# Kernel optimization log

Hardware: AMD Instinct MI355X
Metric: run time of the kernel (lower is better)

The kernel has to match this reference:

```python
import jax, jax.numpy as jnp
import numpy as np

N_HOPS = 3
VOCAB, D = 100000, 300
B, S, T = 128, 2048, 4
N_CLASSES = 3


def setup_inputs() -> dict:
    key = jax.random.key(0)
    ks = jax.random.split(key, 9)
    return {
        "inputs": jax.random.randint(ks[0], (B, S), 0, VOCAB, dtype=jnp.int64 if jax.config.jax_enable_x64 else jnp.int32),
        "targets": jax.random.randint(ks[1], (B, T), 0, VOCAB, dtype=jnp.int64 if jax.config.jax_enable_x64 else jnp.int32),
        "emb_table": jax.random.normal(ks[2], (VOCAB, D), dtype=jnp.float32) * 0.1,
        "W_att": jax.random.normal(ks[3], (2 * D, 1), dtype=jnp.float32) * 0.05,
        "b_att": jax.random.normal(ks[4], (1,), dtype=jnp.float32) * 0.05,
        "W_tr": jax.random.normal(ks[5], (D, D), dtype=jnp.float32) * 0.05,
        "b_tr": jax.random.normal(ks[6], (D,), dtype=jnp.float32) * 0.05,
        "W_out": jax.random.normal(ks[7], (D, N_CLASSES), dtype=jnp.float32) * 0.05,
        "b_out": jax.random.normal(ks[8], (N_CLASSES,), dtype=jnp.float32) * 0.05,
    }


def reference(inputs, targets, emb_table, W_att, b_att, W_tr, b_tr, W_out, b_out):
    # Embedding lookups (dropout prob = 0.0 -> identity)
    we = emb_table[inputs]    # [B, S, D] word/context embeddings
    te = emb_table[targets]   # [B, T, D] aspect-term embeddings
    d = we.shape[-1]
    # Split concat-linear: cat([we, u]) @ W_att == we @ Wa + u @ Wu (avoids [B,S,2D] intermediate)
    Wa, Wu = W_att[:d], W_att[d:]          # each [D, 1]
    u = jnp.mean(te, axis=1, keepdims=True)  # [B, 1, D]
    for _ in range(N_HOPS):
        g = jnp.tanh(we @ Wa + u @ Wu + b_att)          # [B, S, 1]
        a = jax.nn.softmax(g, axis=1)                    # softmax over sequence
        vec = jnp.einsum('bs,bsd->bd', a[..., 0], we)    # [B, D] attention-weighted sum
        te = vec[:, None, :] + te @ W_tr + b_tr          # [B, T, D] (broadcast add)
        u = jnp.mean(te, axis=1, keepdims=True)          # [B, 1, D]
    return u[:, 0, :] @ W_out + b_out                    # [B, n_classes]
```

## Files before the change

### kernel.cpp

```cpp
#include <hip/hip_runtime.h>
#include <hip/hip_bf16.h>

#define VOCAB 100000
#define D 300
#define B 128
#define S 2048
#define T 4

#define WS_V      0
#define WS_WTWU   3600
#define WS_WT2WU  3900
#define WS_WTWO   4200
#define WS_W2WO   5100
#define WS_WT3WO  6000
#define WS_CONST  6900
#define WS_DSCAL  6916
#define WS_PROJ   7940


__device__ __forceinline__ float wave_red(float x) {
    #pragma unroll
    for (int m = 1; m < 64; m <<= 1) x += __shfl_xor(x, m, 64);
    return x;
}

__global__ __launch_bounds__(64) void k_derive1(const float* __restrict__ Watt,
                                                const float* __restrict__ Wtr,
                                                const float* __restrict__ Wout,
                                                float* __restrict__ ws) {
    int i = blockIdx.x, lane = threadIdx.x;
    const float* wrow = Wtr + (size_t)i * D;
    float au = 0.f, a0 = 0.f, a1 = 0.f, a2 = 0.f;
    for (int j = lane; j < D; j += 64) {
        float w = wrow[j];
        au += w * Watt[D + j];
        a0 += w * Wout[j * 3 + 0];
        a1 += w * Wout[j * 3 + 1];
        a2 += w * Wout[j * 3 + 2];
    }
    au = wave_red(au); a0 = wave_red(a0); a1 = wave_red(a1); a2 = wave_red(a2);
    if (lane == 0) {
        ws[WS_WTWU + i] = au;
        ws[WS_WTWO + i * 3 + 0] = a0;
        ws[WS_WTWO + i * 3 + 1] = a1;
        ws[WS_WTWO + i * 3 + 2] = a2;
    }
}

__global__ __launch_bounds__(64) void k_derive2(const float* __restrict__ Wtr,
                                                float* __restrict__ ws) {
    int i = blockIdx.x, lane = threadIdx.x;
    const float* wrow = Wtr + (size_t)i * D;
    float au = 0.f, a0 = 0.f, a1 = 0.f, a2 = 0.f;
    for (int j = lane; j < D; j += 64) {
        float w = wrow[j];
        au += w * ws[WS_WTWU + j];
        a0 += w * ws[WS_WTWO + j * 3 + 0];
        a1 += w * ws[WS_WTWO + j * 3 + 1];
        a2 += w * ws[WS_WTWO + j * 3 + 2];
    }
    au = wave_red(au); a0 = wave_red(a0); a1 = wave_red(a1); a2 = wave_red(a2);
    if (lane == 0) {
        ws[WS_WT2WU + i] = au;
        ws[WS_W2WO + i * 3 + 0] = a0;
        ws[WS_W2WO + i * 3 + 1] = a1;
        ws[WS_W2WO + i * 3 + 2] = a2;
    }
}

__global__ __launch_bounds__(64) void k_derive3(const float* __restrict__ Watt,
                                                const float* __restrict__ Wtr,
                                                const float* __restrict__ Wout,
                                                float* __restrict__ ws) {
    int i = blockIdx.x, lane = threadIdx.x;
    const float* wrow = Wtr + (size_t)i * D;
    float a0 = 0.f, a1 = 0.f, a2 = 0.f;
    for (int j = lane; j < D; j += 64) {
        float w = wrow[j];
        a0 += w * ws[WS_W2WO + j * 3 + 0];
        a1 += w * ws[WS_W2WO + j * 3 + 1];
        a2 += w * ws[WS_W2WO + j * 3 + 2];
    }
    a0 = wave_red(a0); a1 = wave_red(a1); a2 = wave_red(a2);
    if (lane == 0) {
        ws[WS_WT3WO + i * 3 + 0] = a0;
        ws[WS_WT3WO + i * 3 + 1] = a1;
        ws[WS_WT3WO + i * 3 + 2] = a2;
    }
    if (lane < 12) {
        float val;
        if      (lane == 0) val = Watt[i];
        else if (lane == 1) val = Watt[D + i];
        else if (lane == 2) val = ws[WS_WTWU + i];
        else if (lane < 6)  val = Wout[i * 3 + (lane - 3)];
        else if (lane < 9)  val = ws[WS_WTWO + i * 3 + (lane - 6)];
        else                val = ws[WS_W2WO + i * 3 + (lane - 9)];
        ws[WS_V + i * 12 + lane] = val;
    }
}

__global__ __launch_bounds__(64) void k_small(const int* __restrict__ targets,
                                              const float* __restrict__ E,
                                              const float* __restrict__ Watt,
                                              const float* __restrict__ Wout,
                                              const float* __restrict__ btr,
                                              float* __restrict__ ws) {
    int lane = threadIdx.x;
    if (blockIdx.x < B) {
        int b = blockIdx.x;
        int t0 = targets[b * T + 0], t1 = targets[b * T + 1];
        int t2 = targets[b * T + 2], t3 = targets[b * T + 3];
        const float* r0 = E + (size_t)t0 * D;
        const float* r1 = E + (size_t)t1 * D;
        const float* r2 = E + (size_t)t2 * D;
        const float* r3 = E + (size_t)t3 * D;
        float a0 = 0.f, a1 = 0.f, a2 = 0.f, a3 = 0.f, a4 = 0.f, a5 = 0.f;
        for (int i = lane; i < D; i += 64) {
            float u = 0.25f * (r0[i] + r1[i] + r2[i] + r3[i]);
            a0 += u * Watt[D + i];
            a1 += u * ws[WS_WTWU + i];
            a2 += u * ws[WS_WT2WU + i];
            a3 += u * ws[WS_WT3WO + i * 3 + 0];
            a4 += u * ws[WS_WT3WO + i * 3 + 1];
            a5 += u * ws[WS_WT3WO + i * 3 + 2];
        }
        a0 = wave_red(a0); a1 = wave_red(a1); a2 = wave_red(a2);
        a3 = wave_red(a3); a4 = wave_red(a4); a5 = wave_red(a5);
        if (lane == 0) {
            float* o = ws + WS_DSCAL + b * 8;
            o[0] = a0; o[1] = a1; o[2] = a2; o[3] = a3; o[4] = a4; o[5] = a5;
        }
    } else {
        float acc[11];
        #pragma unroll
        for (int k = 0; k < 11; ++k) acc[k] = 0.f;
        for (int i = lane; i < D; i += 64) {
            float bt = btr[i];
            acc[0] += bt * Watt[D + i];
            acc[1] += bt * ws[WS_WTWU + i];
            acc[2] += bt * Wout[i * 3 + 0];
            acc[3] += bt * Wout[i * 3 + 1];
            acc[4] += bt * Wout[i * 3 + 2];
            acc[5] += bt * ws[WS_WTWO + i * 3 + 0];
            acc[6] += bt * ws[WS_WTWO + i * 3 + 1];
            acc[7] += bt * ws[WS_WTWO + i * 3 + 2];
            acc[8] += bt * ws[WS_W2WO + i * 3 + 0];
            acc[9] += bt * ws[WS_W2WO + i * 3 + 1];
            acc[10] += bt * ws[WS_W2WO + i * 3 + 2];
        }
        #pragma unroll
        for (int k = 0; k < 11; ++k) acc[k] = wave_red(acc[k]);
        if (lane == 0) {
            #pragma unroll
            for (int k = 0; k < 11; ++k) ws[WS_CONST + k] = acc[k];
        }
    }
}

__global__ __launch_bounds__(256) void k_proj(const float* __restrict__ E,
                                              const float* __restrict__ Vg,
                                              float* __restrict__ proj) {
    int lane = threadIdx.x & 63;
    int wid  = (blockIdx.x * blockDim.x + threadIdx.x) >> 6;
    int row  = wid * 64 + lane;
    if (row >= VOCAB) return;

    const float4* er = (const float4*)(E + (size_t)row * D);
    float acc[12];
    #pragma unroll
    for (int c = 0; c < 12; ++c) acc[c] = 0.f;

    #pragma unroll 5
    for (int k4 = 0; k4 < 75; ++k4) {
        float4 e = er[k4];
        const float* vp = Vg + k4 * 48;
        #pragma unroll
        for (int c = 0; c < 12; ++c) {
            acc[c] += e.x * vp[c];
            acc[c] += e.y * vp[12 + c];
            acc[c] += e.z * vp[24 + c];
            acc[c] += e.w * vp[36 + c];
        }
    }

    float4* dst = (float4*)(proj + (size_t)row * 12);
    dst[0] = make_float4(acc[0], acc[1], acc[2],  acc[3]);
    dst[1] = make_float4(acc[4], acc[5], acc[6],  acc[7]);
    dst[2] = make_float4(acc[8], acc[9], acc[10], acc[11]);
}

__global__ __launch_bounds__(1024) void k_hops(const int* __restrict__ inputs,
                                               const float* __restrict__ ws,
                                               const float* __restrict__ batt,
                                               const float* __restrict__ bout,
                                               float* __restrict__ out) {
    __shared__ float wred[16][13];
    __shared__ float Ash[13];
    __shared__ float sc[4];
    int b = blockIdx.x, tid = threadIdx.x, wave = tid >> 6, lane = tid & 63;
    const float* proj = ws + WS_PROJ;
    const float* cst  = ws + WS_CONST;
    const float* dsc  = ws + WS_DSCAL + b * 8;
    const int*   inp  = inputs + (size_t)b * S;

    float pv[2][12];
    #pragma unroll
    for (int q = 0; q < 2; ++q) {
        int s = tid + 1024 * q;
        int idx = inp[s];
        const float4* pr = (const float4*)(proj + (size_t)idx * 12);
        float4 x = pr[0], y = pr[1], z = pr[2];
        pv[q][0] = x.x; pv[q][1] = x.y; pv[q][2]  = x.z; pv[q][3]  = x.w;
        pv[q][4] = y.x; pv[q][5] = y.y; pv[q][6]  = y.z; pv[q][7]  = y.w;
        pv[q][8] = z.x; pv[q][9] = z.y; pv[q][10] = z.z; pv[q][11] = z.w;
    }

    if (tid == 0) sc[0] = dsc[0] + batt[0];
    __syncthreads();
    float c = sc[0];

    float o3c0 = 0.f, o3c1 = 0.f, o3c2 = 0.f, uWtWu = 0.f;

    #pragma unroll
    for (int hop = 0; hop < 3; ++hop) {
        float acc[12];
        #pragma unroll
        for (int k = 0; k < 12; ++k) acc[k] = 0.f;
        #pragma unroll
        for (int q = 0; q < 2; ++q) {
            float g = tanhf(pv[q][0] + c);
            float e = __expf(g);
            acc[11] += e;
            #pragma unroll
            for (int k = 1; k < 12; ++k) acc[k - 1] += e * pv[q][k];
        }
        #pragma unroll
        for (int m = 1; m < 64; m <<= 1) {
            #pragma unroll
            for (int k = 0; k < 12; ++k) acc[k] += __shfl_xor(acc[k], m, 64);
        }
        if (lane == 0) {
            #pragma unroll
            for (int k = 0; k < 12; ++k) wred[wave][k] = acc[k];
        }
        __syncthreads();
        if (tid < 12) {
            float s = 0.f;
            #pragma unroll
            for (int w = 0; w < 16; ++w) s += wred[w][tid];
            Ash[tid] = s;
        }
        __syncthreads();
        if (tid == 0) {
            float inv = 1.0f / Ash[11];
            if (hop == 0) {
                o3c0  = Ash[8] * inv + dsc[3] + cst[8];
                o3c1  = Ash[9] * inv + dsc[4] + cst[9];
                o3c2  = Ash[10] * inv + dsc[5] + cst[10];
                uWtWu = Ash[1] * inv + dsc[2] + cst[1];
                sc[0] = Ash[0] * inv + dsc[1] + cst[0] + batt[0];
            } else if (hop == 1) {
                o3c0  = Ash[5] * inv + o3c0 + cst[5];
                o3c1  = Ash[6] * inv + o3c1 + cst[6];
                o3c2  = Ash[7] * inv + o3c2 + cst[7];
                sc[0] = Ash[0] * inv + uWtWu + cst[0] + batt[0];
            } else {
                out[b * 3 + 0] = Ash[2] * inv + o3c0 + cst[2] + bout[0];
                out[b * 3 + 1] = Ash[3] * inv + o3c1 + cst[3] + bout[1];
                out[b * 3 + 2] = Ash[4] * inv + o3c2 + cst[4] + bout[2];
            }
        }
        __syncthreads();
        c = sc[0];
    }
}

extern "C" void kernel_launch(void* const* d_in, const int* in_sizes, int n_in,
                              void* d_out, int out_size, void* d_ws, size_t ws_size,
                              hipStream_t stream) {
    const int*   inputs  = (const int*)  d_in[0];
    const int*   targets = (const int*)  d_in[1];
    const float* emb     = (const float*)d_in[2];
    const float* Watt    = (const float*)d_in[3];
    const float* batt    = (const float*)d_in[4];
    const float* Wtr     = (const float*)d_in[5];
    const float* btr     = (const float*)d_in[6];
    const float* Wout    = (const float*)d_in[7];
    const float* bout    = (const float*)d_in[8];
    float* ws  = (float*)d_ws;
    float* out = (float*)d_out;

    hipLaunchKernelGGL(k_derive1, dim3(D),    dim3(64),   0, stream, Watt, Wtr, Wout, ws);
    hipLaunchKernelGGL(k_derive2, dim3(D),    dim3(64),   0, stream, Wtr, ws);
    hipLaunchKernelGGL(k_derive3, dim3(D),    dim3(64),   0, stream, Watt, Wtr, Wout, ws);
    hipLaunchKernelGGL(k_proj,    dim3(391),  dim3(256),  0, stream, emb, ws + WS_V, ws + WS_PROJ);
    hipLaunchKernelGGL(k_small,   dim3(B + 1), dim3(64),  0, stream, targets, emb, Watt, Wout, btr, ws);
    hipLaunchKernelGGL(k_hops,    dim3(B),    dim3(1024), 0, stream, inputs, ws, batt, bout, out);
}
```

Measured before the change: 235.9 us.

## Fuse target-embedding dot products into hop kernel and merge small kernels

```diff
diff --git a/kernel.cpp b/kernel.cpp
--- a/kernel.cpp
+++ b/kernel.cpp
@@ -14,7 +14,6 @@
 #define WS_W2WO   5100
 #define WS_WT3WO  6000
 #define WS_CONST  6900
-#define WS_DSCAL  6916
 #define WS_PROJ   7940
 
 
@@ -22,6 +21,11 @@
     #pragma unroll
     for (int m = 1; m < 64; m <<= 1) x += __shfl_xor(x, m, 64);
     return x;
+}
+
+__device__ __forceinline__ float fast_tanh(float x) {
+    float e = __expf(2.0f * x);
+    return 1.0f - 2.0f / (e + 1.0f);
 }
 
 __global__ __launch_bounds__(64) void k_derive1(const float* __restrict__ Watt,
@@ -47,7 +51,9 @@
     }
 }
 
-__global__ __launch_bounds__(64) void k_derive2(const float* __restrict__ Wtr,
+__global__ __launch_bounds__(64) void k_derive2(const float* __restrict__ Watt,
+                                                const float* __restrict__ Wtr,
+                                                const float* __restrict__ Wout,
                                                 float* __restrict__ ws) {
     int i = blockIdx.x, lane = threadIdx.x;
     const float* wrow = Wtr + (size_t)i * D;
@@ -66,69 +72,41 @@
         ws[WS_W2WO + i * 3 + 1] = a1;
         ws[WS_W2WO + i * 3 + 2] = a2;
     }
+    if (lane < 12) {
+        float val;
+        if      (lane == 0)  val = Watt[i];
+        else if (lane == 1)  val = Watt[D + i];
+        else if (lane == 2)  val = ws[WS_WTWU + i];
+        else if (lane < 6)   val = Wout[i * 3 + (lane - 3)];
+        else if (lane < 9)   val = ws[WS_WTWO + i * 3 + (lane - 6)];
+        else if (lane == 9)  val = a0;
+        else if (lane == 10) val = a1;
+        else                 val = a2;
+        ws[WS_V + i * 12 + lane] = val;
+    }
 }
 
 __global__ __launch_bounds__(64) void k_derive3(const float* __restrict__ Watt,
                                                 const float* __restrict__ Wtr,
                                                 const float* __restrict__ Wout,
+                                                const float* __restrict__ btr,
                                                 float* __restrict__ ws) {
-    int i = blockIdx.x, lane = threadIdx.x;
-    const float* wrow = Wtr + (size_t)i * D;
-    float a0 = 0.f, a1 = 0.f, a2 = 0.f;
-    for (int j = lane; j < D; j += 64) {
-        float w = wrow[j];
-        a0 += w * ws[WS_W2WO + j * 3 + 0];
-        a1 += w * ws[WS_W2WO + j * 3 + 1];
-        a2 += w * ws[WS_W2WO + j * 3 + 2];
-    }
-    a0 = wave_red(a0); a1 = wave_red(a1); a2 = wave_red(a2);
-    if (lane == 0) {
-        ws[WS_WT3WO + i * 3 + 0] = a0;
-        ws[WS_WT3WO + i * 3 + 1] = a1;
-        ws[WS_WT3WO + i * 3 + 2] = a2;
-    }
-    if (lane < 12) {
-        float val;
-        if      (lane == 0) val = Watt[i];
-        else if (lane == 1) val = Watt[D + i];
-        else if (lane == 2) val = ws[WS_WTWU + i];
-        else if (lane < 6)  val = Wout[i * 3 + (lane - 3)];
-        else if (lane < 9)  val = ws[WS_WTWO + i * 3 + (lane - 6)];
-        else                val = ws[WS_W2WO + i * 3 + (lane - 9)];
-        ws[WS_V + i * 12 + lane] = val;
-    }
-}
-
-__global__ __launch_bounds__(64) void k_small(const int* __restrict__ targets,
-                                              const float* __restrict__ E,
-                                              const float* __restrict__ Watt,
-                                              const float* __restrict__ Wout,
-                                              const float* __restrict__ btr,
-                                              float* __restrict__ ws) {
     int lane = threadIdx.x;
-    if (blockIdx.x < B) {
-        int b = blockIdx.x;
-        int t0 = targets[b * T + 0], t1 = targets[b * T + 1];
-        int t2 = targets[b * T + 2], t3 = targets[b * T + 3];
-        const float* r0 = E + (size_t)t0 * D;
-        const float* r1 = E + (size_t)t1 * D;
-        const float* r2 = E + (size_t)t2 * D;
-        const float* r3 = E + (size_t)t3 * D;
-        float a0 = 0.f, a1 = 0.f, a2 = 0.f, a3 = 0.f, a4 = 0.f, a5 = 0.f;
-        for (int i = lane; i < D; i += 64) {
-            float u = 0.25f * (r0[i] + r1[i] + r2[i] + r3[i]);
-            a0 += u * Watt[D + i];
-            a1 += u * ws[WS_WTWU + i];
-            a2 += u * ws[WS_WT2WU + i];
-            a3 += u * ws[WS_WT3WO + i * 3 + 0];
-            a4 += u * ws[WS_WT3WO + i * 3 + 1];
-            a5 += u * ws[WS_WT3WO + i * 3 + 2];
+    if (blockIdx.x < D) {
+        int i = blockIdx.x;
+        const float* wrow = Wtr + (size_t)i * D;
+        float a0 = 0.f, a1 = 0.f, a2 = 0.f;
+        for (int j = lane; j < D; j += 64) {
+            float w = wrow[j];
+            a0 += w * ws[WS_W2WO + j * 3 + 0];
+            a1 += w * ws[WS_W2WO + j * 3 + 1];
+            a2 += w * ws[WS_W2WO + j * 3 + 2];
         }
         a0 = wave_red(a0); a1 = wave_red(a1); a2 = wave_red(a2);
-        a3 = wave_red(a3); a4 = wave_red(a4); a5 = wave_red(a5);
         if (lane == 0) {
-            float* o = ws + WS_DSCAL + b * 8;
-            o[0] = a0; o[1] = a1; o[2] = a2; o[3] = a3; o[4] = a4; o[5] = a5;
+            ws[WS_WT3WO + i * 3 + 0] = a0;
+            ws[WS_WT3WO + i * 3 + 1] = a1;
+            ws[WS_WT3WO + i * 3 + 2] = a2;
         }
     } else {
         float acc[11];
@@ -136,16 +114,16 @@
         for (int k = 0; k < 11; ++k) acc[k] = 0.f;
         for (int i = lane; i < D; i += 64) {
             float bt = btr[i];
-            acc[0] += bt * Watt[D + i];
-            acc[1] += bt * ws[WS_WTWU + i];
-            acc[2] += bt * Wout[i * 3 + 0];
-            acc[3] += bt * Wout[i * 3 + 1];
-            acc[4] += bt * Wout[i * 3 + 2];
-            acc[5] += bt * ws[WS_WTWO + i * 3 + 0];
-            acc[6] += bt * ws[WS_WTWO + i * 3 + 1];
-            acc[7] += bt * ws[WS_WTWO + i * 3 + 2];
-            acc[8] += bt * ws[WS_W2WO + i * 3 + 0];
-            acc[9] += bt * ws[WS_W2WO + i * 3 + 1];
+            acc[0]  += bt * Watt[D + i];
+            acc[1]  += bt * ws[WS_WTWU + i];
+            acc[2]  += bt * Wout[i * 3 + 0];
+            acc[3]  += bt * Wout[i * 3 + 1];
+            acc[4]  += bt * Wout[i * 3 + 2];
+            acc[5]  += bt * ws[WS_WTWO + i * 3 + 0];
+            acc[6]  += bt * ws[WS_WTWO + i * 3 + 1];
+            acc[7]  += bt * ws[WS_WTWO + i * 3 + 2];
+            acc[8]  += bt * ws[WS_W2WO + i * 3 + 0];
+            acc[9]  += bt * ws[WS_W2WO + i * 3 + 1];
             acc[10] += bt * ws[WS_W2WO + i * 3 + 2];
         }
         #pragma unroll
@@ -170,7 +148,7 @@
     #pragma unroll
     for (int c = 0; c < 12; ++c) acc[c] = 0.f;
 
-    #pragma unroll 5
+    #pragma unroll 15
     for (int k4 = 0; k4 < 75; ++k4) {
         float4 e = er[k4];
         const float* vp = Vg + k4 * 48;
@@ -190,17 +168,19 @@
 }
 
 __global__ __launch_bounds__(1024) void k_hops(const int* __restrict__ inputs,
+                                               const int* __restrict__ targets,
+                                               const float* __restrict__ E,
                                                const float* __restrict__ ws,
                                                const float* __restrict__ batt,
                                                const float* __restrict__ bout,
                                                float* __restrict__ out) {
     __shared__ float wred[16][13];
     __shared__ float Ash[13];
+    __shared__ float dsc[8];
     __shared__ float sc[4];
     int b = blockIdx.x, tid = threadIdx.x, wave = tid >> 6, lane = tid & 63;
     const float* proj = ws + WS_PROJ;
     const float* cst  = ws + WS_CONST;
-    const float* dsc  = ws + WS_DSCAL + b * 8;
     const int*   inp  = inputs + (size_t)b * S;
 
     float pv[2][12];
@@ -215,9 +195,74 @@
         pv[q][8] = z.x; pv[q][9] = z.y; pv[q][10] = z.z; pv[q][11] = z.w;
     }
 
-    if (tid == 0) sc[0] = dsc[0] + batt[0];
+    if (wave < 6) {
+        const int* tg = targets + b * T;
+        const float* r0 = E + (size_t)tg[0] * D;
+        const float* r1 = E + (size_t)tg[1] * D;
+        const float* r2 = E + (size_t)tg[2] * D;
+        const float* r3 = E + (size_t)tg[3] * D;
+        const float* vec;
+        int stride3 = 0, col = 0;
+        if      (wave == 0) vec = batt ? nullptr : nullptr;
+        const float* Watt_u = nullptr;
+        float s = 0.f;
+        for (int i = lane; i < D; i += 64) {
+            float u = 0.25f * (r0[i] + r1[i] + r2[i] + r3[i]);
+            float x;
+            if      (wave == 0) x = ws[WS_WTWU - 3600 + 3300 + i];
+            else x = 0.f;
+            (void)x; (void)vec; (void)stride3; (void)col; (void)Watt_u;
+            float v;
+            switch (wave) {
+                case 0: v = *(ws + WS_WTWU + i - 300 + 300); v = 0.f; break;
+                default: v = 0.f;
+            }
+            (void)v;
+            float w;
+            if      (wave == 0) w = ws[3600 + i] * 0.f;
+            else w = 0.f;
+            (void)w;
+            s += 0.f;
+            if      (wave == 0) s += u * ws[WS_WTWU - WS_WTWU + 0];
+            (void)u;
+        }
+        s = 0.f;
+        for (int i = lane; i < D; i += 64) {
+            float u = 0.25f * (r0[i] + r1[i] + r2[i] + r3[i]);
+            float v;
+            if      (wave == 0) v = ws[WS_WTWU + i] * 0.f + *(ws + WS_WTWU + i) * 0.f + 0.f;
+            if      (wave == 0) v = *(E + 0) * 0.f;
+            if      (wave == 0) v = __ldg(ws + WS_WTWU + i) * 0.f;
+            v = 0.f;
+            if      (wave == 0) v = ws[WS_WTWU + i];
+            else if (wave == 1) v = ws[WS_WT2WU + i];
+            else if (wave == 2) v = ws[WS_WT3WO + i * 3 + 0];
+            else if (wave == 3) v = ws[WS_WT3WO + i * 3 + 1];
+            else if (wave == 4) v = ws[WS_WT3WO + i * 3 + 2];
+            else                v = 0.f;
+            s += u * v;
+        }
+        if (wave == 5) {
+            s = 0.f;
+            for (int i = lane; i < D; i += 64) {
+                float u = 0.25f * (r0[i] + r1[i] + r2[i] + r3[i]);
+                s += u * 0.f;
+            }
+        }
+        s = wave_red(s);
+        if (lane == 0) {
+            int slot;
+            if      (wave == 0) slot = 1;
+            else if (wave == 1) slot = 2;
+            else if (wave == 2) slot = 3;
+            else if (wave == 3) slot = 4;
+            else if (wave == 4) slot = 5;
+            else                slot = 0;
+            dsc[slot] = s;
+        }
+    }
     __syncthreads();
-    float c = sc[0];
+    float c = dsc[0] + batt[0];
 
     float o3c0 = 0.f, o3c1 = 0.f, o3c2 = 0.f, uWtWu = 0.f;
 
@@ -228,7 +273,7 @@
         for (int k = 0; k < 12; ++k) acc[k] = 0.f;
         #pragma unroll
         for (int q = 0; q < 2; ++q) {
-            float g = tanhf(pv[q][0] + c);
+            float g = fast_tanh(pv[q][0] + c);
             float e = __expf(g);
             acc[11] += e;
             #pragma unroll
@@ -275,6 +320,116 @@
     }
 }
 
+
+__global__ __launch_bounds__(1024) void k_hops2(const int* __restrict__ inputs,
+                                                const int* __restrict__ targets,
+                                                const float* __restrict__ E,
+                                                const float* __restrict__ Watt,
+                                                const float* __restrict__ ws,
+                                                const float* __restrict__ batt,
+                                                const float* __restrict__ bout,
+                                                float* __restrict__ out) {
+    __shared__ float wred[16][13];
+    __shared__ float Ash[13];
+    __shared__ float dsc[8];
+    __shared__ float sc[4];
+    int b = blockIdx.x, tid = threadIdx.x, wave = tid >> 6, lane = tid & 63;
+    const float* proj = ws + WS_PROJ;
+    const float* cst  = ws + WS_CONST;
+    const int*   inp  = inputs + (size_t)b * S;
+
+    float pv[2][12];
+    #pragma unroll
+    for (int q = 0; q < 2; ++q) {
+        int s = tid + 1024 * q;
+        int idx = inp[s];
+        const float4* pr = (const float4*)(proj + (size_t)idx * 12);
+        float4 x = pr[0], y = pr[1], z = pr[2];
+        pv[q][0] = x.x; pv[q][1] = x.y; pv[q][2]  = x.z; pv[q][3]  = x.w;
+        pv[q][4] = y.x; pv[q][5] = y.y; pv[q][6]  = y.z; pv[q][7]  = y.w;
+        pv[q][8] = z.x; pv[q][9] = z.y; pv[q][10] = z.z; pv[q][11] = z.w;
+    }
+
+    if (wave < 6) {
+        const int* tg = targets + b * T;
+        const float* r0 = E + (size_t)tg[0] * D;
+        const float* r1 = E + (size_t)tg[1] * D;
+        const float* r2 = E + (size_t)tg[2] * D;
+        const float* r3 = E + (size_t)tg[3] * D;
+        float s = 0.f;
+        for (int i = lane; i < D; i += 64) {
+            float u = 0.25f * (r0[i] + r1[i] + r2[i] + r3[i]);
+            float v;
+            if      (wave == 0) v = Watt[D + i];
+            else if (wave == 1) v = ws[WS_WTWU + i];
+            else if (wave == 2) v = ws[WS_WT2WU + i];
+            else if (wave == 3) v = ws[WS_WT3WO + i * 3 + 0];
+            else if (wave == 4) v = ws[WS_WT3WO + i * 3 + 1];
+            else                v = ws[WS_WT3WO + i * 3 + 2];
+            s += u * v;
+        }
+        s = wave_red(s);
+        if (lane == 0) dsc[wave] = s;
+    }
+    __syncthreads();
+    float c = dsc[0] + batt[0];
+
+    float o3c0 = 0.f, o3c1 = 0.f, o3c2 = 0.f, uWtWu = 0.f;
+
+    #pragma unroll
+    for (int hop = 0; hop < 3; ++hop) {
+        float acc[12];
+        #pragma unroll
+        for (int k = 0; k < 12; ++k) acc[k] = 0.f;
+        #pragma unroll
+        for (int q = 0; q < 2; ++q) {
+            float g = fast_tanh(pv[q][0] + c);
+            float e = __expf(g);
+            acc[11] += e;
+            #pragma unroll
+            for (int k = 1; k < 12; ++k) acc[k - 1] += e * pv[q][k];
+        }
+        #pragma unroll
+        for (int m = 1; m < 64; m <<= 1) {
+            #pragma unroll
+            for (int k = 0; k < 12; ++k) acc[k] += __shfl_xor(acc[k], m, 64);
+        }
+        if (lane == 0) {
+            #pragma unroll
+            for (int k = 0; k < 12; ++k) wred[wave][k] = acc[k];
+        }
+        __syncthreads();
+        if (tid < 12) {
+            float s = 0.f;
+            #pragma unroll
+            for (int w = 0; w < 16; ++w) s += wred[w][tid];
+            Ash[tid] = s;
+        }
+        __syncthreads();
+        if (tid == 0) {
+            float inv = 1.0f / Ash[11];
+            if (hop == 0) {
+                o3c0  = Ash[8] * inv + dsc[3] + cst[8];
+                o3c1  = Ash[9] * inv + dsc[4] + cst[9];
+                o3c2  = Ash[10] * inv + dsc[5] + cst[10];
+                uWtWu = Ash[1] * inv + dsc[2] + cst[1];
+                sc[0] = Ash[0] * inv + dsc[1] + cst[0] + batt[0];
+            } else if (hop == 1) {
+                o3c0  = Ash[5] * inv + o3c0 + cst[5];
+                o3c1  = Ash[6] * inv + o3c1 + cst[6];
+                o3c2  = Ash[7] * inv + o3c2 + cst[7];
+                sc[0] = Ash[0] * inv + uWtWu + cst[0] + batt[0];
+            } else {
+                out[b * 3 + 0] = Ash[2] * inv + o3c0 + cst[2] + bout[0];
+                out[b * 3 + 1] = Ash[3] * inv + o3c1 + cst[3] + bout[1];
+                out[b * 3 + 2] = Ash[4] * inv + o3c2 + cst[4] + bout[2];
+            }
+        }
+        __syncthreads();
+        c = sc[0];
+    }
+}
+
 extern "C" void kernel_launch(void* const* d_in, const int* in_sizes, int n_in,
                               void* d_out, int out_size, void* d_ws, size_t ws_size,
                               hipStream_t stream) {
@@ -290,10 +445,10 @@
     float* ws  = (float*)d_ws;
     float* out = (float*)d_out;
 
-    hipLaunchKernelGGL(k_derive1, dim3(D),    dim3(64),   0, stream, Watt, Wtr, Wout, ws);
-    hipLaunchKernelGGL(k_derive2, dim3(D),    dim3(64),   0, stream, Wtr, ws);
-    hipLaunchKernelGGL(k_derive3, dim3(D),    dim3(64),   0, stream, Watt, Wtr, Wout, ws);
-    hipLaunchKernelGGL(k_proj,    dim3(391),  dim3(256),  0, stream, emb, ws + WS_V, ws + WS_PROJ);
-    hipLaunchKernelGGL(k_small,   dim3(B + 1), dim3(64),  0, stream, targets, emb, Watt, Wout, btr, ws);
-    hipLaunchKernelGGL(k_hops,    dim3(B),    dim3(1024), 0, stream, inputs, ws, batt, bout, out);
-}
+    hipLaunchKernelGGL(k_derive1, dim3(D),     dim3(64),   0, stream, Watt, Wtr, Wout, ws);
+    hipLaunchKernelGGL(k_derive2, dim3(D),     dim3(64),   0, stream, Watt, Wtr, Wout, ws);
+    hipLaunchKernelGGL(k_derive3, dim3(D + 1), dim3(64),   0, stream, Watt, Wtr, Wout, btr, ws);
+    hipLaunchKernelGGL(k_proj,    dim3(391),   dim3(256),  0, stream, emb, ws + WS_V, ws + WS_PROJ);
+    hipLaunchKernelGGL(k_hops2,   dim3(B),     dim3(1024), 0, stream, inputs, targets, emb, Watt,
+                       ws, batt, bout, out);
+}
```

Result: slower. 242.9 us (+3.0%).

## Stage embedding tiles in LDS for projection and fold small kernels into neighbors

Applied to the files above, without the earlier changes.

```diff
diff --git a/kernel.cpp b/kernel.cpp
--- a/kernel.cpp
+++ b/kernel.cpp
@@ -14,7 +14,6 @@
 #define WS_W2WO   5100
 #define WS_WT3WO  6000
 #define WS_CONST  6900
-#define WS_DSCAL  6916
 #define WS_PROJ   7940
 
 
@@ -22,6 +21,11 @@
     #pragma unroll
     for (int m = 1; m < 64; m <<= 1) x += __shfl_xor(x, m, 64);
     return x;
+}
+
+__device__ __forceinline__ float fast_tanh(float x) {
+    float e = __expf(2.0f * x);
+    return 1.0f - 2.0f / (e + 1.0f);
 }
 
 __global__ __launch_bounds__(64) void k_derive1(const float* __restrict__ Watt,
@@ -47,7 +51,9 @@
     }
 }
 
-__global__ __launch_bounds__(64) void k_derive2(const float* __restrict__ Wtr,
+__global__ __launch_bounds__(64) void k_derive2(const float* __restrict__ Watt,
+                                                const float* __restrict__ Wtr,
+                                                const float* __restrict__ Wout,
                                                 float* __restrict__ ws) {
     int i = blockIdx.x, lane = threadIdx.x;
     const float* wrow = Wtr + (size_t)i * D;
@@ -66,69 +72,41 @@
         ws[WS_W2WO + i * 3 + 1] = a1;
         ws[WS_W2WO + i * 3 + 2] = a2;
     }
+    if (lane < 12) {
+        float val;
+        if      (lane == 0)  val = Watt[i];
+        else if (lane == 1)  val = Watt[D + i];
+        else if (lane == 2)  val = ws[WS_WTWU + i];
+        else if (lane < 6)   val = Wout[i * 3 + (lane - 3)];
+        else if (lane < 9)   val = ws[WS_WTWO + i * 3 + (lane - 6)];
+        else if (lane == 9)  val = a0;
+        else if (lane == 10) val = a1;
+        else                 val = a2;
+        ws[WS_V + i * 12 + lane] = val;
+    }
 }
 
 __global__ __launch_bounds__(64) void k_derive3(const float* __restrict__ Watt,
                                                 const float* __restrict__ Wtr,
                                                 const float* __restrict__ Wout,
+                                                const float* __restrict__ btr,
                                                 float* __restrict__ ws) {
-    int i = blockIdx.x, lane = threadIdx.x;
-    const float* wrow = Wtr + (size_t)i * D;
-    float a0 = 0.f, a1 = 0.f, a2 = 0.f;
-    for (int j = lane; j < D; j += 64) {
-        float w = wrow[j];
-        a0 += w * ws[WS_W2WO + j * 3 + 0];
-        a1 += w * ws[WS_W2WO + j * 3 + 1];
-        a2 += w * ws[WS_W2WO + j * 3 + 2];
-    }
-    a0 = wave_red(a0); a1 = wave_red(a1); a2 = wave_red(a2);
-    if (lane == 0) {
-        ws[WS_WT3WO + i * 3 + 0] = a0;
-        ws[WS_WT3WO + i * 3 + 1] = a1;
-        ws[WS_WT3WO + i * 3 + 2] = a2;
-    }
-    if (lane < 12) {
-        float val;
-        if      (lane == 0) val = Watt[i];
-        else if (lane == 1) val = Watt[D + i];
-        else if (lane == 2) val = ws[WS_WTWU + i];
-        else if (lane < 6)  val = Wout[i * 3 + (lane - 3)];
-        else if (lane < 9)  val = ws[WS_WTWO + i * 3 + (lane - 6)];
-        else                val = ws[WS_W2WO + i * 3 + (lane - 9)];
-        ws[WS_V + i * 12 + lane] = val;
-    }
-}
-
-__global__ __launch_bounds__(64) void k_small(const int* __restrict__ targets,
-                                              const float* __restrict__ E,
-                                              const float* __restrict__ Watt,
-                                              const float* __restrict__ Wout,
-                                              const float* __restrict__ btr,
-                                              float* __restrict__ ws) {
     int lane = threadIdx.x;
-    if (blockIdx.x < B) {
-        int b = blockIdx.x;
-        int t0 = targets[b * T + 0], t1 = targets[b * T + 1];
-        int t2 = targets[b * T + 2], t3 = targets[b * T + 3];
-        const float* r0 = E + (size_t)t0 * D;
-        const float* r1 = E + (size_t)t1 * D;
-        const float* r2 = E + (size_t)t2 * D;
-        const float* r3 = E + (size_t)t3 * D;
-        float a0 = 0.f, a1 = 0.f, a2 = 0.f, a3 = 0.f, a4 = 0.f, a5 = 0.f;
-        for (int i = lane; i < D; i += 64) {
-            float u = 0.25f * (r0[i] + r1[i] + r2[i] + r3[i]);
-            a0 += u * Watt[D + i];
-            a1 += u * ws[WS_WTWU + i];
-            a2 += u * ws[WS_WT2WU + i];
-            a3 += u * ws[WS_WT3WO + i * 3 + 0];
-            a4 += u * ws[WS_WT3WO + i * 3 + 1];
-            a5 += u * ws[WS_WT3WO + i * 3 + 2];
+    if (blockIdx.x < D) {
+        int i = blockIdx.x;
+        const float* wrow = Wtr + (size_t)i * D;
+        float a0 = 0.f, a1 = 0.f, a2 = 0.f;
+        for (int j = lane; j < D; j += 64) {
+            float w = wrow[j];
+            a0 += w * ws[WS_W2WO + j * 3 + 0];
+            a1 += w * ws[WS_W2WO + j * 3 + 1];
+            a2 += w * ws[WS_W2WO + j * 3 + 2];
         }
         a0 = wave_red(a0); a1 = wave_red(a1); a2 = wave_red(a2);
-        a3 = wave_red(a3); a4 = wave_red(a4); a5 = wave_red(a5);
         if (lane == 0) {
-            float* o = ws + WS_DSCAL + b * 8;
-            o[0] = a0; o[1] = a1; o[2] = a2; o[3] = a3; o[4] = a4; o[5] = a5;
+            ws[WS_WT3WO + i * 3 + 0] = a0;
+            ws[WS_WT3WO + i * 3 + 1] = a1;
+            ws[WS_WT3WO + i * 3 + 2] = a2;
         }
     } else {
         float acc[11];
@@ -136,16 +114,16 @@
         for (int k = 0; k < 11; ++k) acc[k] = 0.f;
         for (int i = lane; i < D; i += 64) {
             float bt = btr[i];
-            acc[0] += bt * Watt[D + i];
-            acc[1] += bt * ws[WS_WTWU + i];
-            acc[2] += bt * Wout[i * 3 + 0];
-            acc[3] += bt * Wout[i * 3 + 1];
-            acc[4] += bt * Wout[i * 3 + 2];
-            acc[5] += bt * ws[WS_WTWO + i * 3 + 0];
-            acc[6] += bt * ws[WS_WTWO + i * 3 + 1];
-            acc[7] += bt * ws[WS_WTWO + i * 3 + 2];
-            acc[8] += bt * ws[WS_W2WO + i * 3 + 0];
-            acc[9] += bt * ws[WS_W2WO + i * 3 + 1];
+            acc[0]  += bt * Watt[D + i];
+            acc[1]  += bt * ws[WS_WTWU + i];
+            acc[2]  += bt * Wout[i * 3 + 0];
+            acc[3]  += bt * Wout[i * 3 + 1];
+            acc[4]  += bt * Wout[i * 3 + 2];
+            acc[5]  += bt * ws[WS_WTWO + i * 3 + 0];
+            acc[6]  += bt * ws[WS_WTWO + i * 3 + 1];
+            acc[7]  += bt * ws[WS_WTWO + i * 3 + 2];
+            acc[8]  += bt * ws[WS_W2WO + i * 3 + 0];
+            acc[9]  += bt * ws[WS_W2WO + i * 3 + 1];
             acc[10] += bt * ws[WS_W2WO + i * 3 + 2];
         }
         #pragma unroll
@@ -160,47 +138,66 @@
 __global__ __launch_bounds__(256) void k_proj(const float* __restrict__ E,
                                               const float* __restrict__ Vg,
                                               float* __restrict__ proj) {
-    int lane = threadIdx.x & 63;
-    int wid  = (blockIdx.x * blockDim.x + threadIdx.x) >> 6;
-    int row  = wid * 64 + lane;
-    if (row >= VOCAB) return;
-
-    const float4* er = (const float4*)(E + (size_t)row * D);
+    __shared__ float4 sbuf[256 * 16];
+    const int tid   = threadIdx.x;
+    const int R0    = blockIdx.x * 256;
+    const int myrow = R0 + tid;
+    const float4* E4 = (const float4*)E;
+
     float acc[12];
     #pragma unroll
     for (int c = 0; c < 12; ++c) acc[c] = 0.f;
 
-    #pragma unroll 5
-    for (int k4 = 0; k4 < 75; ++k4) {
-        float4 e = er[k4];
-        const float* vp = Vg + k4 * 48;
-        #pragma unroll
-        for (int c = 0; c < 12; ++c) {
-            acc[c] += e.x * vp[c];
-            acc[c] += e.y * vp[12 + c];
-            acc[c] += e.z * vp[24 + c];
-            acc[c] += e.w * vp[36 + c];
-        }
-    }
-
-    float4* dst = (float4*)(proj + (size_t)row * 12);
-    dst[0] = make_float4(acc[0], acc[1], acc[2],  acc[3]);
-    dst[1] = make_float4(acc[4], acc[5], acc[6],  acc[7]);
-    dst[2] = make_float4(acc[8], acc[9], acc[10], acc[11]);
+    for (int ch = 0; ch < 5; ++ch) {
+        #pragma unroll
+        for (int j = 0; j < 15; ++j) {
+            int L = tid + j * 256;
+            int r = L / 15;
+            int m = L - r * 15;
+            float4 v = make_float4(0.f, 0.f, 0.f, 0.f);
+            int gr = R0 + r;
+            if (gr < VOCAB) v = E4[(size_t)gr * 75 + ch * 15 + m];
+            sbuf[r * 16 + (m ^ (r & 15))] = v;
+        }
+        __syncthreads();
+        if (myrow < VOCAB) {
+            #pragma unroll
+            for (int m = 0; m < 15; ++m) {
+                float4 e = sbuf[tid * 16 + (m ^ (tid & 15))];
+                const float* vp = Vg + (ch * 60 + m * 4) * 12;
+                #pragma unroll
+                for (int c = 0; c < 12; ++c) {
+                    acc[c] += e.x * vp[c]      + e.y * vp[12 + c]
+                            + e.z * vp[24 + c] + e.w * vp[36 + c];
+                }
+            }
+        }
+        __syncthreads();
+    }
+
+    if (myrow < VOCAB) {
+        float4* dst = (float4*)(proj + (size_t)myrow * 12);
+        dst[0] = make_float4(acc[0], acc[1], acc[2],  acc[3]);
+        dst[1] = make_float4(acc[4], acc[5], acc[6],  acc[7]);
+        dst[2] = make_float4(acc[8], acc[9], acc[10], acc[11]);
+    }
 }
 
 __global__ __launch_bounds__(1024) void k_hops(const int* __restrict__ inputs,
+                                               const int* __restrict__ targets,
+                                               const float* __restrict__ E,
+                                               const float* __restrict__ Watt,
                                                const float* __restrict__ ws,
                                                const float* __restrict__ batt,
                                                const float* __restrict__ bout,
                                                float* __restrict__ out) {
     __shared__ float wred[16][13];
     __shared__ float Ash[13];
+    __shared__ float dsc[8];
     __shared__ float sc[4];
     int b = blockIdx.x, tid = threadIdx.x, wave = tid >> 6, lane = tid & 63;
     const float* proj = ws + WS_PROJ;
     const float* cst  = ws + WS_CONST;
-    const float* dsc  = ws + WS_DSCAL + b * 8;
     const int*   inp  = inputs + (size_t)b * S;
 
     float pv[2][12];
@@ -215,9 +212,29 @@
         pv[q][8] = z.x; pv[q][9] = z.y; pv[q][10] = z.z; pv[q][11] = z.w;
     }
 
-    if (tid == 0) sc[0] = dsc[0] + batt[0];
+    if (wave < 6) {
+        const int* tg = targets + b * T;
+        const float* r0 = E + (size_t)tg[0] * D;
+        const float* r1 = E + (size_t)tg[1] * D;
+        const float* r2 = E + (size_t)tg[2] * D;
+        const float* r3 = E + (size_t)tg[3] * D;
+        float s = 0.f;
+        for (int i = lane; i < D; i += 64) {
+            float u = 0.25f * (r0[i] + r1[i] + r2[i] + r3[i]);
+            float v;
+            if      (wave == 0) v = Watt[D + i];
+            else if (wave == 1) v = ws[WS_WTWU + i];
+            else if (wave == 2) v = ws[WS_WT2WU + i];
+            else if (wave == 3) v = ws[WS_WT3WO + i * 3 + 0];
+            else if (wave == 4) v = ws[WS_WT3WO + i * 3 + 1];
+            else                v = ws[WS_WT3WO + i * 3 + 2];
+            s += u * v;
+        }
+        s = wave_red(s);
+        if (lane == 0) dsc[wave] = s;
+    }
     __syncthreads();
-    float c = sc[0];
+    float c = dsc[0] + batt[0];
 
     float o3c0 = 0.f, o3c1 = 0.f, o3c2 = 0.f, uWtWu = 0.f;
 
@@ -228,7 +245,7 @@
         for (int k = 0; k < 12; ++k) acc[k] = 0.f;
         #pragma unroll
         for (int q = 0; q < 2; ++q) {
-            float g = tanhf(pv[q][0] + c);
+            float g = fast_tanh(pv[q][0] + c);
             float e = __expf(g);
             acc[11] += e;
             #pragma unroll
@@ -290,10 +307,10 @@
     float* ws  = (float*)d_ws;
     float* out = (float*)d_out;
 
-    hipLaunchKernelGGL(k_derive1, dim3(D),    dim3(64),   0, stream, Watt, Wtr, Wout, ws);
-    hipLaunchKernelGGL(k_derive2, dim3(D),    dim3(64),   0, stream, Wtr, ws);
-    hipLaunchKernelGGL(k_derive3, dim3(D),    dim3(64),   0, stream, Watt, Wtr, Wout, ws);
-    hipLaunchKernelGGL(k_proj,    dim3(391),  dim3(256),  0, stream, emb, ws + WS_V, ws + WS_PROJ);
-    hipLaunchKernelGGL(k_small,   dim3(B + 1), dim3(64),  0, stream, targets, emb, Watt, Wout, btr, ws);
-    hipLaunchKernelGGL(k_hops,    dim3(B),    dim3(1024), 0, stream, inputs, ws, batt, bout, out);
-}
+    hipLaunchKernelGGL(k_derive1, dim3(D),     dim3(64),   0, stream, Watt, Wtr, Wout, ws);
+    hipLaunchKernelGGL(k_derive2, dim3(D),     dim3(64),   0, stream, Watt, Wtr, Wout, ws);
+    hipLaunchKernelGGL(k_derive3, dim3(D + 1), dim3(64),   0, stream, Watt, Wtr, Wout, btr, ws);
+    hipLaunchKernelGGL(k_proj,    dim3(391),   dim3(256),  0, stream, emb, ws + WS_V, ws + WS_PROJ);
+    hipLaunchKernelGGL(k_hops,    dim3(B),     dim3(1024), 0, stream, inputs, targets, emb, Watt,
+                       ws, batt, bout, out);
+}
```

After: 255.7 us. 1.08x slower.
